# Performance work log

Measured on AMD Instinct MI355X. Metric: run time of the kernel, lower is better.

The kernel has to match this reference:

```python
import jax, jax.numpy as jnp
import numpy as np

D_MODEL, N_HEADS, HEAD_DIM, MAX_POS = 1536, 16, 96, 4096
B, T = 2, 2048
BASE = 10000.0


def build_rope3d_Rs(head_dim, max_pos, base=BASE):
    """Rodrigues rotations R(t) = exp(t*M_k): (max_pos, n_trip, 3, 3)."""
    n_trip = head_dim // 3
    inv_freq = base ** (-np.arange(n_trip, dtype=np.float64) * 2.0 / head_dim)
    Ms = np.zeros((n_trip, 3, 3), dtype=np.float64)
    for k in range(n_trip):  # tiny fixed loop (n_trip=32)
        m, axis = inv_freq[k], k % 3
        if axis == 0:
            Ms[k, 0, 1], Ms[k, 1, 0] = m, -m
        elif axis == 1:
            Ms[k, 1, 2], Ms[k, 2, 1] = m, -m
        else:
            Ms[k, 0, 2], Ms[k, 2, 0] = m, -m
    m_s = np.abs(Ms).max(axis=(1, 2))                      # (n_trip,)
    pos = np.arange(max_pos, dtype=np.float64)
    ang = pos[:, None] * m_s[None, :]                      # (P, n_trip)
    Mu = Ms / np.maximum(m_s, 1e-30)[:, None, None]
    Mu2 = np.einsum('kij,kjl->kil', Mu, Mu)
    Rs = (np.eye(3)[None, None]
          + np.sin(ang)[..., None, None] * Mu[None]
          + (1.0 - np.cos(ang))[..., None, None] * Mu2[None])
    return jnp.asarray(Rs, dtype=jnp.float32)


def setup_inputs() -> dict:
    key = jax.random.key(0)
    kx, kq, ko = jax.random.split(key, 3)
    s_in = 1.0 / np.sqrt(D_MODEL)
    s_out = 1.0 / np.sqrt(N_HEADS * HEAD_DIM)
    return {
        'x': jax.random.normal(kx, (B, T, D_MODEL), dtype=jnp.float32),
        'w_qkv': jax.random.normal(kq, (3 * N_HEADS * HEAD_DIM, D_MODEL), dtype=jnp.float32) * s_in,
        'w_o': jax.random.normal(ko, (D_MODEL, N_HEADS * HEAD_DIM), dtype=jnp.float32) * s_out,
        'Rs': build_rope3d_Rs(HEAD_DIM, MAX_POS),
    }


def apply_rope3d(x, Rs):
    # x: (B,H,T,d); Rs: (P, n_trip, 3, 3), d = 3*n_trip
    b, h, t, d = x.shape
    xg = x.reshape(b, h, t, d // 3, 3)
    out = jnp.einsum('tkij,bhtkj->bhtki', Rs[:t], xg)
    return out.reshape(b, h, t, d)


def reference(x, w_qkv, w_o, Rs):
    b, t, _ = x.shape
    qkv = (x @ w_qkv.T).reshape(b, t, 3, N_HEADS, HEAD_DIM)
    qkv = jnp.transpose(qkv, (2, 0, 3, 1, 4))              # (3,B,H,T,hd)
    q, k, v = qkv[0], qkv[1], qkv[2]
    q = apply_rope3d(q, Rs)
    k = apply_rope3d(k, Rs)
    scale = 1.0 / jnp.sqrt(jnp.asarray(HEAD_DIM, dtype=x.dtype))
    scores = jnp.einsum('bhqd,bhkd->bhqk', q, k) * scale   # (B,H,T,T)
    causal = jnp.tril(jnp.ones((t, t), dtype=bool))
    scores = jnp.where(causal, scores, jnp.finfo(x.dtype).min)
    att = jax.nn.softmax(scores, axis=-1)
    out = jnp.einsum('bhqk,bhkd->bhqd', att, v)            # (B,H,T,hd)
    out = jnp.transpose(out, (0, 2, 1, 3)).reshape(b, t, N_HEADS * HEAD_DIM)
    return out @ w_o.T
```

## Files before the change

### kernel.cpp

```cpp
#include <hip/hip_runtime.h>
#include <stdint.h>


typedef unsigned short u16;
typedef unsigned int u32;
typedef __attribute__((ext_vector_type(8))) __bf16 bf16x8;
typedef __attribute__((ext_vector_type(4))) float f32x4;

#define DEV static __device__ __forceinline__

DEV u16 f2bf(float f) {
  u32 u = __float_as_uint(f);
  return (u16)((u + 0x7fffu + ((u >> 16) & 1u)) >> 16);
}
DEV float bf2f(u16 h) { return __uint_as_float(((u32)h) << 16); }
DEV u32 cvtpk(float lo, float hi) {
  u32 r;
  asm("v_cvt_pk_bf16_f32 %0, %1, %2" : "=v"(r) : "v"(lo), "v"(hi));
  return r;
}
DEV float exp2f_fast(float x) {
  float r;
  asm("v_exp_f32 %0, %1" : "=v"(r) : "v"(x));
  return r;
}

DEV void gload16(u16* lds_dst, const u16* gsrc) {
  __builtin_amdgcn_global_load_lds(
      (const __attribute__((address_space(1))) void*)gsrc,
      (__attribute__((address_space(3))) void*)lds_dst, 16, 0, 0);
}

__global__ __launch_bounds__(256) void cvt_bf16(const float* __restrict__ in,
                                                u16* __restrict__ out, int n4) {
  int i = blockIdx.x * 256 + threadIdx.x;
  if (i < n4) {
    float4 v = reinterpret_cast<const float4*>(in)[i];
    ushort4 o;
    o.x = f2bf(v.x); o.y = f2bf(v.y); o.z = f2bf(v.z); o.w = f2bf(v.w);
    reinterpret_cast<ushort4*>(out)[i] = o;
  }
}

template <int OUT_BF16>
__global__ __launch_bounds__(256) void gemm_bt(const u16* __restrict__ A,
                                               const u16* __restrict__ B,
                                               void* __restrict__ Cv,
                                               int M, int N, int K) {
  __shared__ __align__(16) u16 lA[128 * 32];
  __shared__ __align__(16) u16 lB[128 * 32];
  const int tid = threadIdx.x;
  const int lane = tid & 63;
  const int w = tid >> 6;
  const int wr = (w >> 1) * 64;
  const int wc = (w & 1) * 64;
  const int fr = lane & 15;
  const int fq = lane >> 4;
  const int row0 = blockIdx.x * 128;
  const int col0 = blockIdx.y * 128;

  const f32x4 z4 = {0.f, 0.f, 0.f, 0.f};
  f32x4 acc[4][4];
#pragma unroll
  for (int m = 0; m < 4; ++m)
#pragma unroll
    for (int n = 0; n < 4; ++n) acc[m][n] = z4;

  const int sr = tid >> 2;
  const int sc = (tid & 3) * 8;

  for (int k0 = 0; k0 < K; k0 += 32) {
    __syncthreads();
#pragma unroll
    for (int rep = 0; rep < 2; ++rep) {
      const int row = rep * 64 + sr;
      const int ldsbase = (rep * 256 + w * 64) * 8;
      gload16(lA + ldsbase, A + (size_t)(row0 + row) * K + (k0 + sc));
      gload16(lB + ldsbase, B + (size_t)(col0 + row) * K + (k0 + sc));
    }
    __syncthreads();

    bf16x8 af[4], bfr[4];
#pragma unroll
    for (int m = 0; m < 4; ++m)
      af[m] = *reinterpret_cast<const bf16x8*>(lA + (wr + m * 16 + fr) * 32 + fq * 8);
#pragma unroll
    for (int n = 0; n < 4; ++n)
      bfr[n] = *reinterpret_cast<const bf16x8*>(lB + (wc + n * 16 + fr) * 32 + fq * 8);
#pragma unroll
    for (int m = 0; m < 4; ++m)
#pragma unroll
      for (int n = 0; n < 4; ++n)
        acc[m][n] = __builtin_amdgcn_mfma_f32_16x16x32_bf16(af[m], bfr[n], acc[m][n], 0, 0, 0);
  }

#pragma unroll
  for (int m = 0; m < 4; ++m) {
    const int grow0 = row0 + wr + m * 16 + fq * 4;
#pragma unroll
    for (int n = 0; n < 4; ++n) {
      const int gcol = col0 + wc + n * 16 + fr;
#pragma unroll
      for (int j = 0; j < 4; ++j) {
        const size_t off = (size_t)(grow0 + j) * N + gcol;
        if (OUT_BF16) ((u16*)Cv)[off] = f2bf(acc[m][n][j]);
        else          ((float*)Cv)[off] = acc[m][n][j];
      }
    }
  }
}

__global__ __launch_bounds__(256) void rope_kernel(u16* __restrict__ qkv,
                                                   const float* __restrict__ Rs) {
  const int bid = blockIdx.x;
  const int qk = bid & 1;
  const int bt = bid >> 1;
  const int t = bt & 2047;
  const int tid = threadIdx.x;

  __shared__ __align__(16) u16 buf[1536];
  __shared__ __align__(16) float rbuf[288];

  u16* g = qkv + (size_t)bt * 4608 + qk * 1536;
  if (tid < 192)
    *reinterpret_cast<uint4*>(buf + tid * 8) = *reinterpret_cast<const uint4*>(g + tid * 8);
  if (tid < 72)
    *reinterpret_cast<float4*>(rbuf + tid * 4) =
        *reinterpret_cast<const float4*>(Rs + (size_t)t * 288 + tid * 4);
  __syncthreads();

#pragma unroll
  for (int rep = 0; rep < 2; ++rep) {
    const int ft = rep * 256 + tid;
    const int base = (ft >> 5) * 96 + (ft & 31) * 3;
    const float* R = rbuf + (ft & 31) * 9;
    const float x0 = bf2f(buf[base]), x1 = bf2f(buf[base + 1]), x2 = bf2f(buf[base + 2]);
    const float y0 = R[0] * x0 + R[1] * x1 + R[2] * x2;
    const float y1 = R[3] * x0 + R[4] * x1 + R[5] * x2;
    const float y2 = R[6] * x0 + R[7] * x1 + R[8] * x2;
    buf[base] = f2bf(y0); buf[base + 1] = f2bf(y1); buf[base + 2] = f2bf(y2);
  }
  __syncthreads();
  if (tid < 192)
    *reinterpret_cast<uint4*>(g + tid * 8) = *reinterpret_cast<const uint4*>(buf + tid * 8);
}

__global__ __launch_bounds__(256) void kvprep(const u16* __restrict__ qkv,
                                              u16* __restrict__ Kf,
                                              u16* __restrict__ Vf) {
  const int kt = blockIdx.x, bh = blockIdx.y;
  const int b = bh >> 4, h = bh & 15;
  const int tid = threadIdx.x, lane = tid & 63, w = tid >> 6;
  const float SC = 0.14724574f;
  __shared__ __align__(16) u16 vlds[64 * 96];

#pragma unroll
  for (int r = 0; r < 3; ++r) {
    const int idx = r * 256 + tid;
    const int kv = idx / 12, c8 = (idx % 12) * 8;
    gload16(vlds + (r * 256 + w * 64) * 8,
            qkv + (size_t)(b * 2048 + kt * 64 + kv) * 4608 + 3072 + h * 96 + c8);
  }

  const size_t obase = ((size_t)bh * 32 + kt) * 6144;
#pragma unroll
  for (int r = 0; r < 3; ++r) {
    const int chunk = r * 256 + tid;
    const int sub = chunk >> 6, l = chunk & 63;
    const int m = sub / 3, kb = sub % 3;
    const int fr = l & 15, fq = l >> 4;
    uint4 v = *reinterpret_cast<const uint4*>(
        qkv + (size_t)(b * 2048 + kt * 64 + m * 16 + fr) * 4608 + 1536 + h * 96 + kb * 32 + fq * 8);
    u16* p = reinterpret_cast<u16*>(&v);
#pragma unroll
    for (int e = 0; e < 8; ++e) p[e] = f2bf(bf2f(p[e]) * SC);
    *reinterpret_cast<uint4*>(Kf + obase + (size_t)chunk * 8) = v;
  }
  __syncthreads();
#pragma unroll
  for (int r = 0; r < 3; ++r) {
    const int chunk = r * 256 + tid;
    const int sub = chunk >> 6, l = chunk & 63;
    const int n2 = sub >> 1, c = sub & 1;
    const int fr = l & 15, fq = l >> 4;
    const int d = n2 * 16 + fr;
    u16 out[8];
#pragma unroll
    for (int e = 0; e < 8; ++e) {
      const int kl = (c * 2 + (e >> 2)) * 16 + fq * 4 + (e & 3);
      out[e] = vlds[kl * 96 + d];
    }
    *reinterpret_cast<uint4*>(Vf + obase + (size_t)chunk * 8) =
        *reinterpret_cast<uint4*>(out);
  }
}

__global__ __launch_bounds__(256, 2) void attn_fwd(const u16* __restrict__ qkvb,
                                                   const u16* __restrict__ Kf,
                                                   const u16* __restrict__ Vf,
                                                   u16* __restrict__ y) {
  const int bh = blockIdx.x;
  const int qt = 15 - (int)blockIdx.y;
  const int b = bh >> 4, h = bh & 15;
  const int tid = threadIdx.x, lane = tid & 63, w = tid >> 6;
  const int fr = lane & 15, fq = lane >> 4;
  const int q0 = qt * 128;
  const int qw = q0 + w * 32;

  __shared__ __align__(16) u16 kbl[2][6144];
  __shared__ __align__(16) u16 vbl[2][6144];

  bf16x8 qf[2][3];
#pragma unroll
  for (int nq = 0; nq < 2; ++nq)
#pragma unroll
    for (int kb = 0; kb < 3; ++kb)
      qf[nq][kb] = *reinterpret_cast<const bf16x8*>(
          qkvb + (size_t)(b * 2048 + qw + nq * 16 + fr) * 4608 + h * 96 + kb * 32 + fq * 8);

  const f32x4 z4 = {0.f, 0.f, 0.f, 0.f};
  f32x4 oacc[2][6];
#pragma unroll
  for (int mq = 0; mq < 2; ++mq)
#pragma unroll
    for (int n2 = 0; n2 < 6; ++n2) oacc[mq][n2] = z4;
  float mrow[2] = {-1e30f, -1e30f}, ssum[2] = {0.f, 0.f};

  const int nt = 2 * qt + 2;
  const size_t tb = (size_t)bh * 32 * 6144;

#define STAGE(buf, kt_)                                                         \
  do {                                                                          \
    const size_t sb = tb + (size_t)(kt_)*6144;                                  \
    _Pragma("unroll") for (int r = 0; r < 3; ++r) {                             \
      gload16(kbl[buf] + (r * 256 + w * 64) * 8, Kf + sb + (r * 256 + w * 64 + lane) * 8); \
      gload16(vbl[buf] + (r * 256 + w * 64) * 8, Vf + sb + (r * 256 + w * 64 + lane) * 8); \
    }                                                                           \
  } while (0)

  STAGE(0, 0);
  for (int kt = 0; kt < nt; ++kt) {
    __syncthreads();
    if (kt + 1 < nt) STAGE((kt + 1) & 1, kt + 1);
    const u16* kc = kbl[kt & 1];
    const u16* vc = vbl[kt & 1];
    const int k0 = kt * 64;

    if (k0 <= qw + 31) {
      f32x4 sacc[4][2];
#pragma unroll
      for (int m = 0; m < 4; ++m)
#pragma unroll
        for (int nq = 0; nq < 2; ++nq) sacc[m][nq] = z4;
#pragma unroll
      for (int kb = 0; kb < 3; ++kb)
#pragma unroll
        for (int m = 0; m < 4; ++m) {
          const bf16x8 kfrag = *reinterpret_cast<const bf16x8*>(kc + ((m * 3 + kb) * 64 + lane) * 8);
#pragma unroll
          for (int nq = 0; nq < 2; ++nq)
            sacc[m][nq] = __builtin_amdgcn_mfma_f32_16x16x32_bf16(kfrag, qf[nq][kb], sacc[m][nq], 0, 0, 0);
        }
      if (k0 + 63 > qw) {
#pragma unroll
        for (int m = 0; m < 4; ++m) {
          const int kpos = k0 + m * 16 + fq * 4;
#pragma unroll
          for (int nq = 0; nq < 2; ++nq) {
            const int qpos = qw + nq * 16 + fr;
#pragma unroll
            for (int j = 0; j < 4; ++j)
              if (kpos + j > qpos) sacc[m][nq][j] = -1e30f;
          }
        }
      }
      float al[2];
#pragma unroll
      for (int nq = 0; nq < 2; ++nq) {
        float mx = sacc[0][nq][0];
#pragma unroll
        for (int m = 0; m < 4; ++m)
#pragma unroll
          for (int j = 0; j < 4; ++j) mx = fmaxf(mx, sacc[m][nq][j]);
        mx = fmaxf(mx, __shfl_xor(mx, 16));
        mx = fmaxf(mx, __shfl_xor(mx, 32));
        const float mn = fmaxf(mrow[nq], mx);
        al[nq] = exp2f_fast(mrow[nq] - mn);
        mrow[nq] = mn;
        float s = 0.f;
#pragma unroll
        for (int m = 0; m < 4; ++m) {
          f32x4 p;
#pragma unroll
          for (int j = 0; j < 4; ++j) p[j] = exp2f_fast(sacc[m][nq][j] - mn);
          sacc[m][nq] = p;
          s += (p[0] + p[1]) + (p[2] + p[3]);
        }
        s += __shfl_xor(s, 16);
        s += __shfl_xor(s, 32);
        ssum[nq] = ssum[nq] * al[nq] + s;
      }
      float alb[2][4];
#pragma unroll
      for (int mq = 0; mq < 2; ++mq)
#pragma unroll
        for (int j = 0; j < 4; ++j) alb[mq][j] = __shfl(al[mq], fq * 4 + j);
#pragma unroll
      for (int mq = 0; mq < 2; ++mq)
#pragma unroll
        for (int n2 = 0; n2 < 6; ++n2) {
          f32x4 t = oacc[mq][n2];
          t[0] *= alb[mq][0]; t[1] *= alb[mq][1]; t[2] *= alb[mq][2]; t[3] *= alb[mq][3];
          oacc[mq][n2] = t;
        }
      union PB { u32 u[4]; bf16x8 v; };
      PB pa[2][2];
#pragma unroll
      for (int c = 0; c < 2; ++c)
#pragma unroll
        for (int mq = 0; mq < 2; ++mq) {
          pa[c][mq].u[0] = cvtpk(sacc[2 * c][mq][0], sacc[2 * c][mq][1]);
          pa[c][mq].u[1] = cvtpk(sacc[2 * c][mq][2], sacc[2 * c][mq][3]);
          pa[c][mq].u[2] = cvtpk(sacc[2 * c + 1][mq][0], sacc[2 * c + 1][mq][1]);
          pa[c][mq].u[3] = cvtpk(sacc[2 * c + 1][mq][2], sacc[2 * c + 1][mq][3]);
        }
#pragma unroll
      for (int c = 0; c < 2; ++c)
#pragma unroll
        for (int n2 = 0; n2 < 6; ++n2) {
          const bf16x8 vfrag = *reinterpret_cast<const bf16x8*>(vc + ((n2 * 2 + c) * 64 + lane) * 8);
#pragma unroll
          for (int mq = 0; mq < 2; ++mq)
            oacc[mq][n2] = __builtin_amdgcn_mfma_f32_16x16x32_bf16(pa[c][mq].v, vfrag, oacc[mq][n2], 0, 0, 0);
        }
    }
  }
#undef STAGE

  float inv[2][4];
#pragma unroll
  for (int mq = 0; mq < 2; ++mq)
#pragma unroll
    for (int j = 0; j < 4; ++j)
      inv[mq][j] = __builtin_amdgcn_rcpf(__shfl(ssum[mq], fq * 4 + j));
#pragma unroll
  for (int mq = 0; mq < 2; ++mq)
#pragma unroll
    for (int n2 = 0; n2 < 6; ++n2)
#pragma unroll
      for (int j = 0; j < 4; ++j) {
        const size_t off =
            (size_t)(b * 2048 + qw + mq * 16 + fq * 4 + j) * 1536 + h * 96 + n2 * 16 + fr;
        y[off] = f2bf(oacc[mq][n2][j] * inv[mq][j]);
      }
}

extern "C" void kernel_launch(void* const* d_in, const int* in_sizes, int n_in,
                              void* d_out, int out_size, void* d_ws, size_t ws_size,
                              hipStream_t stream) {
  (void)in_sizes; (void)n_in; (void)out_size; (void)ws_size;
  const float* x     = (const float*)d_in[0];
  const float* w_qkv = (const float*)d_in[1];
  const float* w_o   = (const float*)d_in[2];
  const float* Rs    = (const float*)d_in[3];
  float* out = (float*)d_out;

  u16* xb    = (u16*)d_ws;
  u16* wqkvb = xb + 6291456;
  u16* wob   = xb + 13369344;
  u16* qkvb  = xb + 15728640;
  u16* yb    = xb + 34603008;
  u16* Kf    = xb;
  u16* Vf    = xb + 6291456;

  cvt_bf16<<<1572864 / 256, 256, 0, stream>>>(x, xb, 1572864);
  cvt_bf16<<<1769472 / 256, 256, 0, stream>>>(w_qkv, wqkvb, 1769472);
  cvt_bf16<<<589824 / 256, 256, 0, stream>>>(w_o, wob, 589824);

  gemm_bt<1><<<dim3(32, 36), 256, 0, stream>>>(xb, wqkvb, (void*)qkvb, 4096, 4608, 1536);
  rope_kernel<<<8192, 256, 0, stream>>>(qkvb, Rs);
  kvprep<<<dim3(32, 32), 256, 0, stream>>>(qkvb, Kf, Vf);
  attn_fwd<<<dim3(32, 16), 256, 0, stream>>>(qkvb, Kf, Vf, yb);
  gemm_bt<0><<<dim3(32, 12), 256, 0, stream>>>(yb, wob, (void*)out, 4096, 1536, 1536);
}
```

Before: 328.2 us.

## Replace QKV projection GEMM with 256x256-tile double-buffered 512-thread kernel

Adds a new bf16 GEMM kernel with 256x256 output tiles, 8 waves, XOR-swizzled LDS and double-buffered global-to-LDS loads interleaved with MFMA phases, and uses it for the QKV projection. Larger tiles raise data reuse per LDS load and overlap the next K-slab prefetch with compute. The grid shrinks to 288 blocks, which may underfill the 256 CUs with a tail wave, and the large LDS footprint (128KB) limits occupancy.

```diff
diff --git a/kernel.cpp b/kernel.cpp
--- a/kernel.cpp
+++ b/kernel.cpp
@@ -110,6 +110,127 @@
   }
 }
 
+template <int OUT_BF16>
+__global__ __launch_bounds__(512, 2) void gemm256(const u16* __restrict__ A,
+                                                  const u16* __restrict__ B,
+                                                  void* __restrict__ Cv,
+                                                  int M, int N, int K) {
+  __shared__ __align__(16) u16 sA[2][16384];
+  __shared__ __align__(16) u16 sB[2][16384];
+  const int tid = threadIdx.x;
+  const int lane = tid & 63, w = tid >> 6;
+  const int wm = w >> 2, wn = w & 3;
+  const int fr = lane & 15, fq = lane >> 4;
+  const int r0 = blockIdx.x * 256, c0 = blockIdx.y * 256;
+
+  const u16* aSrc[4];
+  const u16* bSrc[4];
+#pragma unroll
+  for (int c = 0; c < 4; ++c) {
+    const int idx = c * 512 + tid;
+    const int row = idx >> 3;
+    const int col = ((idx & 7) ^ (row & 7)) * 8;
+    aSrc[c] = A + (size_t)(r0 + row) * K + col;
+    bSrc[c] = B + (size_t)(c0 + row) * K + col;
+  }
+
+  const int sw0 = ((fq) ^ (fr & 7)) * 8;
+  const int sw1 = ((4 + fq) ^ (fr & 7)) * 8;
+  const int aB = wm * 8192 + fr * 64;
+  const int bB = wn * 4096 + fr * 64;
+
+  const f32x4 z4 = {0.f, 0.f, 0.f, 0.f};
+  f32x4 acc[8][4];
+#pragma unroll
+  for (int m = 0; m < 8; ++m)
+#pragma unroll
+    for (int n = 0; n < 4; ++n) acc[m][n] = z4;
+
+  const int NT = K >> 6;
+
+#define SG(arr, src, c, buf, ko) \
+  gload16(&arr[buf][(c * 512 + w * 64) * 8], src[c] + (ko))
+
+  SG(sB, bSrc, 0, 0, 0); SG(sB, bSrc, 1, 0, 0);
+  SG(sB, bSrc, 2, 0, 0); SG(sB, bSrc, 3, 0, 0);
+  SG(sA, aSrc, 0, 0, 0); SG(sA, aSrc, 2, 0, 0);
+  SG(sA, aSrc, 1, 0, 0); SG(sA, aSrc, 3, 0, 0);
+
+  for (int u = 0; u < NT; ++u) {
+    const int par = u & 1, nxt = par ^ 1;
+    const u16* a = sA[par];
+    const u16* b = sB[par];
+    const bool pf = (u + 1 < NT);
+    const size_t ko = (size_t)(u + 1) * 64;
+    bf16x8 bf[4][2], af[2][2];
+
+#define RD_A(p)                                                              \
+  _Pragma("unroll") for (int i = 0; i < 2; ++i) {                            \
+    af[i][0] = *(const bf16x8*)(a + aB + (2 * (p) + i) * 1024 + sw0);        \
+    af[i][1] = *(const bf16x8*)(a + aB + (2 * (p) + i) * 1024 + sw1);        \
+  }
+#define MM(p)                                                                \
+  __builtin_amdgcn_s_setprio(1);                                             \
+  _Pragma("unroll") for (int i = 0; i < 2; ++i)                              \
+  _Pragma("unroll") for (int n = 0; n < 4; ++n)                              \
+  _Pragma("unroll") for (int ks = 0; ks < 2; ++ks)                           \
+    acc[2 * (p) + i][n] = __builtin_amdgcn_mfma_f32_16x16x32_bf16(           \
+        af[i][ks], bf[n][ks], acc[2 * (p) + i][n], 0, 0, 0);                 \
+  __builtin_amdgcn_s_setprio(0);
+
+    asm volatile("s_waitcnt vmcnt(2)" ::: "memory");
+    __builtin_amdgcn_s_barrier();
+#pragma unroll
+    for (int n = 0; n < 4; ++n) {
+      bf[n][0] = *(const bf16x8*)(b + bB + n * 1024 + sw0);
+      bf[n][1] = *(const bf16x8*)(b + bB + n * 1024 + sw1);
+    }
+    RD_A(0)
+    if (pf) { SG(sB, bSrc, 0, nxt, ko); SG(sB, bSrc, 1, nxt, ko); }
+    __builtin_amdgcn_s_barrier();
+    MM(0)
+    __builtin_amdgcn_s_barrier();
+
+    RD_A(1)
+    if (pf) { SG(sB, bSrc, 2, nxt, ko); SG(sB, bSrc, 3, nxt, ko); }
+    __builtin_amdgcn_s_barrier();
+    MM(1)
+    __builtin_amdgcn_s_barrier();
+
+    if (pf) { asm volatile("s_waitcnt vmcnt(4)" ::: "memory"); }
+    else    { asm volatile("s_waitcnt vmcnt(0)" ::: "memory"); }
+    RD_A(2)
+    if (pf) { SG(sA, aSrc, 0, nxt, ko); SG(sA, aSrc, 2, nxt, ko); }
+    __builtin_amdgcn_s_barrier();
+    MM(2)
+    __builtin_amdgcn_s_barrier();
+
+    RD_A(3)
+    if (pf) { SG(sA, aSrc, 1, nxt, ko); SG(sA, aSrc, 3, nxt, ko); }
+    __builtin_amdgcn_s_barrier();
+    MM(3)
+    __builtin_amdgcn_s_barrier();
+#undef RD_A
+#undef MM
+  }
+#undef SG
+
+#pragma unroll
+  for (int m = 0; m < 8; ++m) {
+    const int gr = r0 + wm * 128 + m * 16 + fq * 4;
+#pragma unroll
+    for (int n = 0; n < 4; ++n) {
+      const int gc = c0 + wn * 64 + n * 16 + fr;
+#pragma unroll
+      for (int j = 0; j < 4; ++j) {
+        const size_t off = (size_t)(gr + j) * N + gc;
+        if (OUT_BF16) ((u16*)Cv)[off] = f2bf(acc[m][n][j]);
+        else          ((float*)Cv)[off] = acc[m][n][j];
+      }
+    }
+  }
+}
+
 __global__ __launch_bounds__(256) void rope_kernel(u16* __restrict__ qkv,
                                                    const float* __restrict__ Rs) {
   const int bid = blockIdx.x;
@@ -377,7 +498,7 @@
   cvt_bf16<<<1769472 / 256, 256, 0, stream>>>(w_qkv, wqkvb, 1769472);
   cvt_bf16<<<589824 / 256, 256, 0, stream>>>(w_o, wob, 589824);
 
-  gemm_bt<1><<<dim3(32, 36), 256, 0, stream>>>(xb, wqkvb, (void*)qkvb, 4096, 4608, 1536);
+  gemm256<1><<<dim3(16, 18), 512, 0, stream>>>(xb, wqkvb, (void*)qkvb, 4096, 4608, 1536);
   rope_kernel<<<8192, 256, 0, stream>>>(qkvb, Rs);
   kvprep<<<dim3(32, 32), 256, 0, stream>>>(qkvb, Kf, Vf);
   attn_fwd<<<dim3(32, 16), 256, 0, stream>>>(qkvb, Kf, Vf, yb);
```

New measurement: 330.6 us. About the same (+0.7%).

## Rewrite GEMM with double-buffered swizzled LDS and 128x192 tiles

Applied to the files above, without the earlier changes.

Replaces the simple single-buffered 128x128 GEMM with a 512-thread kernel that uses 128x192 tiles, a K-step of 64, double-buffered LDS with async global-to-LDS prefetch of the next tile, and an XOR swizzle on LDS rows to avoid bank conflicts. The goal is to hide global memory latency behind MFMA work and lower LDS traffic per flop in both projection GEMMs. The change raises LDS use to about 80KB per block and relies on hand-placed vmcnt waits and barriers, so an ordering mistake could race. Grid sizes change so that N divides by 192.

```diff
diff --git a/kernel.cpp b/kernel.cpp
--- a/kernel.cpp
+++ b/kernel.cpp
@@ -43,66 +43,108 @@
 }
 
 template <int OUT_BF16>
-__global__ __launch_bounds__(256) void gemm_bt(const u16* __restrict__ A,
-                                               const u16* __restrict__ B,
-                                               void* __restrict__ Cv,
-                                               int M, int N, int K) {
-  __shared__ __align__(16) u16 lA[128 * 32];
-  __shared__ __align__(16) u16 lB[128 * 32];
+__global__ __launch_bounds__(512, 4) void gemm_bal(const u16* __restrict__ A,
+                                                   const u16* __restrict__ B,
+                                                   void* __restrict__ Cv,
+                                                   int M, int N, int K) {
+  (void)M;
+  __shared__ __align__(16) u16 sA[2][128 * 64];
+  __shared__ __align__(16) u16 sB[2][192 * 64];
   const int tid = threadIdx.x;
-  const int lane = tid & 63;
-  const int w = tid >> 6;
-  const int wr = (w >> 1) * 64;
-  const int wc = (w & 1) * 64;
-  const int fr = lane & 15;
-  const int fq = lane >> 4;
-  const int row0 = blockIdx.x * 128;
-  const int col0 = blockIdx.y * 128;
+  const int lane = tid & 63, w = tid >> 6;
+  const int wm = w >> 2, wn = w & 3;
+  const int fr = lane & 15, fq = lane >> 4;
+  const int r0 = blockIdx.x * 128, c0 = blockIdx.y * 192;
+
+  const u16* aSrc[2];
+  const u16* bSrc[3];
+#pragma unroll
+  for (int c = 0; c < 2; ++c) {
+    const int idx = c * 512 + tid;
+    const int row = idx >> 3;
+    aSrc[c] = A + (size_t)(r0 + row) * K + ((idx & 7) ^ (row & 7)) * 8;
+  }
+#pragma unroll
+  for (int c = 0; c < 3; ++c) {
+    const int idx = c * 512 + tid;
+    const int row = idx >> 3;
+    bSrc[c] = B + (size_t)(c0 + row) * K + ((idx & 7) ^ (row & 7)) * 8;
+  }
+
+  const int sw0 = ((fq) ^ (fr & 7)) * 8;
+  const int sw1 = ((4 + fq) ^ (fr & 7)) * 8;
+  const int aB = (wm * 64 + fr) * 64;
+  const int bB = (wn * 48 + fr) * 64;
 
   const f32x4 z4 = {0.f, 0.f, 0.f, 0.f};
-  f32x4 acc[4][4];
+  f32x4 acc[4][3];
 #pragma unroll
   for (int m = 0; m < 4; ++m)
 #pragma unroll
-    for (int n = 0; n < 4; ++n) acc[m][n] = z4;
-
-  const int sr = tid >> 2;
-  const int sc = (tid & 3) * 8;
-
-  for (int k0 = 0; k0 < K; k0 += 32) {
-    __syncthreads();
-#pragma unroll
-    for (int rep = 0; rep < 2; ++rep) {
-      const int row = rep * 64 + sr;
-      const int ldsbase = (rep * 256 + w * 64) * 8;
-      gload16(lA + ldsbase, A + (size_t)(row0 + row) * K + (k0 + sc));
-      gload16(lB + ldsbase, B + (size_t)(col0 + row) * K + (k0 + sc));
+    for (int n = 0; n < 3; ++n) acc[m][n] = z4;
+
+  const int NT = K >> 6;
+
+#define SGA(c, buf, ko) gload16(&sA[buf][((c)*512 + w * 64) * 8], aSrc[c] + (ko))
+#define SGB(c, buf, ko) gload16(&sB[buf][((c)*512 + w * 64) * 8], bSrc[c] + (ko))
+
+  SGA(0, 0, 0); SGA(1, 0, 0);
+  SGB(0, 0, 0); SGB(1, 0, 0); SGB(2, 0, 0);
+
+  for (int u = 0; u < NT; ++u) {
+    const int par = u & 1, nxt = par ^ 1;
+    const u16* a = sA[par];
+    const u16* b = sB[par];
+    const bool pf = (u + 1 < NT);
+    const size_t ko = (size_t)(u + 1) * 64;
+
+    asm volatile("s_waitcnt vmcnt(3)" ::: "memory");
+    __builtin_amdgcn_s_barrier();
+    if (pf) { SGA(0, nxt, ko); SGA(1, nxt, ko); }
+
+    if (pf) { asm volatile("s_waitcnt vmcnt(2)" ::: "memory"); }
+    else    { asm volatile("s_waitcnt vmcnt(0)" ::: "memory"); }
+    __builtin_amdgcn_s_barrier();
+    bf16x8 bfr[3][2];
+#pragma unroll
+    for (int n = 0; n < 3; ++n) {
+      bfr[n][0] = *(const bf16x8*)(b + bB + n * 1024 + sw0);
+      bfr[n][1] = *(const bf16x8*)(b + bB + n * 1024 + sw1);
     }
-    __syncthreads();
-
-    bf16x8 af[4], bfr[4];
-#pragma unroll
-    for (int m = 0; m < 4; ++m)
-      af[m] = *reinterpret_cast<const bf16x8*>(lA + (wr + m * 16 + fr) * 32 + fq * 8);
-#pragma unroll
-    for (int n = 0; n < 4; ++n)
-      bfr[n] = *reinterpret_cast<const bf16x8*>(lB + (wc + n * 16 + fr) * 32 + fq * 8);
-#pragma unroll
-    for (int m = 0; m < 4; ++m)
-#pragma unroll
-      for (int n = 0; n < 4; ++n)
-        acc[m][n] = __builtin_amdgcn_mfma_f32_16x16x32_bf16(af[m], bfr[n], acc[m][n], 0, 0, 0);
-  }
+    if (pf) { SGB(0, nxt, ko); SGB(1, nxt, ko); SGB(2, nxt, ko); }
+    __builtin_amdgcn_s_barrier();
+    __builtin_amdgcn_s_setprio(1);
+#pragma unroll
+    for (int mp = 0; mp < 2; ++mp) {
+      bf16x8 afr[2][2];
+#pragma unroll
+      for (int i = 0; i < 2; ++i) {
+        afr[i][0] = *(const bf16x8*)(a + aB + (2 * mp + i) * 1024 + sw0);
+        afr[i][1] = *(const bf16x8*)(a + aB + (2 * mp + i) * 1024 + sw1);
+      }
+#pragma unroll
+      for (int i = 0; i < 2; ++i)
+#pragma unroll
+        for (int n = 0; n < 3; ++n)
+#pragma unroll
+          for (int ks = 0; ks < 2; ++ks)
+            acc[2 * mp + i][n] = __builtin_amdgcn_mfma_f32_16x16x32_bf16(
+                afr[i][ks], bfr[n][ks], acc[2 * mp + i][n], 0, 0, 0);
+    }
+    __builtin_amdgcn_s_setprio(0);
+  }
+#undef SGA
+#undef SGB
 
 #pragma unroll
   for (int m = 0; m < 4; ++m) {
-    const int grow0 = row0 + wr + m * 16 + fq * 4;
-#pragma unroll
-    for (int n = 0; n < 4; ++n) {
-      const int gcol = col0 + wc + n * 16 + fr;
+    const int gr = r0 + wm * 64 + m * 16 + fq * 4;
+#pragma unroll
+    for (int n = 0; n < 3; ++n) {
+      const int gc = c0 + wn * 48 + n * 16 + fr;
 #pragma unroll
       for (int j = 0; j < 4; ++j) {
-        const size_t off = (size_t)(grow0 + j) * N + gcol;
+        const size_t off = (size_t)(gr + j) * N + gc;
         if (OUT_BF16) ((u16*)Cv)[off] = f2bf(acc[m][n][j]);
         else          ((float*)Cv)[off] = acc[m][n][j];
       }
@@ -377,9 +419,9 @@
   cvt_bf16<<<1769472 / 256, 256, 0, stream>>>(w_qkv, wqkvb, 1769472);
   cvt_bf16<<<589824 / 256, 256, 0, stream>>>(w_o, wob, 589824);
 
-  gemm_bt<1><<<dim3(32, 36), 256, 0, stream>>>(xb, wqkvb, (void*)qkvb, 4096, 4608, 1536);
+  gemm_bal<1><<<dim3(32, 24), 512, 0, stream>>>(xb, wqkvb, (void*)qkvb, 4096, 4608, 1536);
   rope_kernel<<<8192, 256, 0, stream>>>(qkvb, Rs);
   kvprep<<<dim3(32, 32), 256, 0, stream>>>(qkvb, Kf, Vf);
   attn_fwd<<<dim3(32, 16), 256, 0, stream>>>(qkvb, Kf, Vf, yb);
-  gemm_bt<0><<<dim3(32, 12), 256, 0, stream>>>(yb, wob, (void*)out, 4096, 1536, 1536);
-}
+  gemm_bal<0><<<dim3(32, 8), 512, 0, stream>>>(yb, wob, (void*)out, 4096, 1536, 1536);
+}
```

After: 295.3 us. -10.0%, faster.
